# Optimization experiments

Hardware: AMD Instinct MI355X
Metric: run time of the kernel (lower is better)

The kernel has to match this reference:

```python
import jax, jax.numpy as jnp
import numpy as np

HIDDEN = 64
N_NODES = 100000
N_EDGES = 1250000
EDGE_FEAT = 13


def setup_inputs() -> dict:
    key = jax.random.key(0)
    ks = jax.random.split(key, 16)
    d = HIDDEN
    inp = {
        'x': jax.random.normal(ks[0], (N_NODES, d), dtype=jnp.float32),
        'edge_index': jax.random.randint(ks[1], (2, N_EDGES), 0, N_NODES, dtype=jnp.int64),
        'edge_attr': jax.random.uniform(ks[2], (N_EDGES, EDGE_FEAT), dtype=jnp.float32),
        # learned params
        'aaaaa': jax.random.normal(ks[3], (EDGE_FEAT, 1), dtype=jnp.float32) * 0.5,
        'W1': jax.random.normal(ks[4], (d, d), dtype=jnp.float32) / np.sqrt(d),
        'b1': jnp.zeros((d,), dtype=jnp.float32),
        'W2': jax.random.normal(ks[5], (d, d), dtype=jnp.float32) / np.sqrt(d),
        'b2': jnp.zeros((d,), dtype=jnp.float32),
        'W3': jax.random.normal(ks[6], (d, d), dtype=jnp.float32) / np.sqrt(d),
        'b3': jnp.zeros((d,), dtype=jnp.float32),
        'wg1': jax.random.normal(ks[7], (d, 1), dtype=jnp.float32) / np.sqrt(d),
        'bg1': jnp.zeros((1,), dtype=jnp.float32),
        'wg2': jax.random.normal(ks[8], (d, 1), dtype=jnp.float32) / np.sqrt(d),
        'bg2': jnp.zeros((1,), dtype=jnp.float32),
        'wg3': jax.random.normal(ks[9], (d, 1), dtype=jnp.float32) / np.sqrt(d),
        'bg3': jnp.zeros((1,), dtype=jnp.float32),
    }
    return inp


def _gcn_norm(edge_index, edge_weight, num_nodes):
    # PyG gcn_norm: add self-loops (weight 1), symmetric deg^{-1/2} normalization
    loop = jnp.arange(num_nodes, dtype=edge_index.dtype)
    rows = jnp.concatenate([edge_index[0], loop])
    cols = jnp.concatenate([edge_index[1], loop])
    w = jnp.concatenate([edge_weight, jnp.ones((num_nodes,), edge_weight.dtype)])
    deg = jax.ops.segment_sum(w, cols, num_segments=num_nodes)
    dinv = jnp.where(deg > 0, jax.lax.rsqrt(jnp.where(deg > 0, deg, 1.0)), 0.0)
    norm = dinv[rows] * w * dinv[cols]
    return rows, cols, norm


def _gcn_layer(x, W, b, rows, cols, norm, num_nodes):
    h = x @ W  # transform first (out_dim == in_dim)
    msg = norm[:, None] * h[rows]          # gather + scale  [E+N, d]
    out = jnp.zeros_like(h).at[cols].add(msg)  # scatter-add aggregation
    return out + b


def _att_pool(x, wg, bg):
    # GlobalAttention with single graph (batch all zeros):
    # gate = sigmoid(Linear(x)); softmax over nodes; weighted sum
    gate = jax.nn.sigmoid(x @ wg + bg)      # [N, 1]
    a = jax.nn.softmax(gate, axis=0)        # softmax over node dim
    return jnp.sum(a * x, axis=0, keepdims=True)  # [1, d]


def reference(x, edge_index, edge_attr, aaaaa, W1, b1, W2, b2, W3, b3,
              wg1, bg1, wg2, bg2, wg3, bg3):
    num_nodes = x.shape[0]
    edge_weight = (edge_attr @ jax.nn.softmax(aaaaa, axis=0)).reshape(-1)  # [E]
    rows, cols, norm = _gcn_norm(edge_index, edge_weight, num_nodes)

    x1 = jax.nn.relu(_gcn_layer(x, W1, b1, rows, cols, norm, num_nodes))
    r1 = _att_pool(x1, wg1, bg1)
    x2 = jax.nn.relu(_gcn_layer(x1, W2, b2, rows, cols, norm, num_nodes))
    r2 = _att_pool(x2, wg2, bg2)
    x3 = jax.nn.relu(_gcn_layer(x2, W3, b3, rows, cols, norm, num_nodes))
    r3 = _att_pool(x3, wg3, bg3)
    return jnp.concatenate([r1, r2, r3], axis=1)  # [1, 3*hidden]
```

## Files before the change

kernel.cpp:

```cpp
#include <hip/hip_runtime.h>
#include <hip/hip_bf16.h>
#include <math.h>

#define HIDDEN    64
#define N_NODES   100000
#define N_EDGES   1250000
#define EDGE_FEAT 13

#define GATHER_BLOCKS 2048
#define GEMM_NB   ((N_NODES + 255) / 256)

#define NBKT    391
#define BCAP    4096
#define A_EPB   512
#define NBLKA   ((N_EDGES + A_EPB - 1) / A_EPB)
#define CPT     ((NBLKA + 255) / 256)

typedef unsigned short bf16_t;
typedef unsigned char  u8;
typedef unsigned short u16;
typedef unsigned int   u32;
typedef unsigned long long u64;
typedef float f32x2 __attribute__((ext_vector_type(2)));

#if defined(__has_builtin)
# if __has_builtin(__builtin_amdgcn_cvt_f32_fp8)
#  define USE_HW_FP8 1
# endif
# if __has_builtin(__builtin_amdgcn_cvt_pk_f32_fp8)
#  define USE_HW_FP8PK 1
# endif
#endif

static __device__ __forceinline__ float bf2f(bf16_t u) {
    union { unsigned int i; float f; } x; x.i = ((unsigned int)u) << 16; return x.f;
}
static __device__ __forceinline__ bf16_t f2bf(float f) {
    union { float f; unsigned int i; } u; u.f = f;
    unsigned int r = u.i + 0x7FFFu + ((u.i >> 16) & 1u);
    return (bf16_t)(r >> 16);
}

static __device__ __forceinline__ u8 f2fp8(float f) {
    union { float f; unsigned int u; } v; v.f = f;
    unsigned int s = (v.u >> 31) << 7;
    unsigned int mag = v.u & 0x7fffffffu;
    if (mag >= 0x43E80000u) return (u8)(s | 0x7Eu);
    if (mag < 0x3C800000u) {
        union { unsigned int u; float f; } t; t.u = mag;
        int qi = (int)rintf(t.f * 512.0f);
        return (u8)(s | (unsigned int)qi);
    }
    unsigned int r = mag + 0x7FFFFu + ((mag >> 20) & 1u);
    unsigned int e8 = (r >> 23) - 120u;
    unsigned int m3 = (r >> 20) & 7u;
    return (u8)(s | (e8 << 3) | m3);
}

static __device__ __forceinline__ float fp8dec(u32 b) {
#ifdef USE_HW_FP8
    return __builtin_amdgcn_cvt_f32_fp8(b, 0);
#else
    u32 m = b & 0x7Fu;
    u32 sgn = (b & 0x80u) << 24;
    union { u32 u; float f; } fn; fn.u = 0x3C000000u + (m << 20);
    float mg = (m < 8u) ? (float)m * (1.0f / 512.0f) : fn.f;
    union { float f; u32 u; } r; r.f = mg; r.u |= sgn;
    return r.f;
#endif
}

static __device__ __forceinline__ void fp8x4dec(u32 w, float* f) {
#ifdef USE_HW_FP8PK
    f32x2 lo = __builtin_amdgcn_cvt_pk_f32_fp8(w, false);
    f32x2 hi = __builtin_amdgcn_cvt_pk_f32_fp8(w, true);
    f[0] = lo.x; f[1] = lo.y; f[2] = hi.x; f[3] = hi.y;
#else
    f[0] = fp8dec(w & 0xFFu);
    f[1] = fp8dec((w >> 8) & 0xFFu);
    f[2] = fp8dec((w >> 16) & 0xFFu);
    f[3] = fp8dec((w >> 24) & 0xFFu);
#endif
}

#define OFF_TOT    0
#define OFF_GBASE  2048
#define OFF_BLKH   4096
#define OFF_BLKE   3824640
#define OFF_VST    7645184
#define OFF_START  7645184
#define OFF_DINV   8045184
#define OFF_ACC    8445184
#define OFF_POOLP  8446208
#define OFF_REC    10043648
#define OFF_H8     17645184
#define OFF_A      24045184
#define OFF_BREC   OFF_H8

__global__ __launch_bounds__(256) void wqk_kernel(
    const float* __restrict__ attr, const int* __restrict__ rows,
    const int* __restrict__ cols, const float* __restrict__ aaaaa,
    u64* __restrict__ vstash, int* __restrict__ blkHist, int E)
{
    __shared__ float s[16];
    __shared__ int hist[NBKT];
    __shared__ float astage[4][EDGE_FEAT * 64];
    int t = threadIdx.x, blk = blockIdx.x;
    int lane = t & 63, wid = t >> 6;
    if (t == 0) {
        float m = -1e30f;
        for (int i = 0; i < EDGE_FEAT; i++) m = fmaxf(m, aaaaa[i]);
        float ex[EDGE_FEAT]; float sum = 0.f;
        for (int i = 0; i < EDGE_FEAT; i++) { ex[i] = __expf(aaaaa[i] - m); sum += ex[i]; }
        float inv = 1.f / sum;
        for (int i = 0; i < EDGE_FEAT; i++) s[i] = ex[i] * inv;
    }
    for (int b = t; b < NBKT; b += 256) hist[b] = 0;
    __syncthreads();

    float sw[EDGE_FEAT];
#pragma unroll
    for (int f = 0; f < EDGE_FEAT; f++) sw[f] = s[f];

    float* as = astage[wid];
    int wbase = blk * A_EPB + wid * (A_EPB / 4);
#pragma unroll 1
    for (int c = 0; c < A_EPB / 4 / 64; c++) {
        int ebase = wbase + c * 64;
        int rem = E - ebase;
        if (rem <= 0) break;
        int limw = min(64, rem) * EDGE_FEAT;
        size_t gb = (size_t)ebase * EDGE_FEAT;
#pragma unroll
        for (int j = 0; j < EDGE_FEAT; j++) {
            int idx = lane + j * 64;
            if (idx < limw) as[idx] = attr[gb + idx];
        }
        int e = ebase + lane;
        if (e < E) {
            const float* rowp = &as[lane * EDGE_FEAT];
            float acc = 0.f;
#pragma unroll
            for (int f = 0; f < EDGE_FEAT; f++) acc = fmaf(rowp[f], sw[f], acc);
            u32 wq = min((u32)(fmaxf(acc, 0.f) * 32768.0f), 32767u);
            u32 cc = (u32)cols[e], rr = (u32)rows[e];
            int rk = atomicAdd(&hist[cc >> 8], 1);
            vstash[e] = ((u64)(u32)rk << 49) | ((u64)wq << 34) | ((u64)cc << 17) | (u64)rr;
        }
    }
    __syncthreads();
    for (int b = t; b < NBKT; b += 256) blkHist[blk * NBKT + b] = hist[b];
}

__global__ __launch_bounds__(256) void colscan_kernel(
    const int* __restrict__ blkHist, int* __restrict__ blkExcl,
    int* __restrict__ bucketTot)
{
    __shared__ int sc[256];
    int t = threadIdx.x, b = blockIdx.x;
    int loc[CPT]; int lsum = 0;
#pragma unroll
    for (int i = 0; i < CPT; i++) {
        int k = t * CPT + i;
        int v = (k < NBLKA) ? blkHist[(size_t)k * NBKT + b] : 0;
        loc[i] = lsum; lsum += v;
    }
    sc[t] = lsum;
    __syncthreads();
    for (int off = 1; off < 256; off <<= 1) {
        int a = (t >= off) ? sc[t - off] : 0;
        __syncthreads();
        sc[t] += a;
        __syncthreads();
    }
    int excl = sc[t] - lsum;
#pragma unroll
    for (int i = 0; i < CPT; i++) {
        int k = t * CPT + i;
        if (k < NBLKA) blkExcl[(size_t)k * NBKT + b] = excl + loc[i];
    }
    if (t == 255) bucketTot[b] = sc[255];
}

__global__ void bscan(const int* __restrict__ bucketTot, int* __restrict__ gbase) {
    __shared__ int sc[512];
    int t = threadIdx.x;
    int v0 = (t < NBKT) ? bucketTot[t] : 0;
    int v1 = (t + 256 < NBKT) ? bucketTot[t + 256] : 0;
    sc[t] = v0; sc[t + 256] = v1;
    __syncthreads();
    for (int off = 1; off < 512; off <<= 1) {
        int a0 = (t >= off) ? sc[t - off] : 0;
        int a1 = sc[t + 256 - off];
        __syncthreads();
        sc[t] += a0; sc[t + 256] += a1;
        __syncthreads();
    }
    if (t < NBKT) gbase[t] = sc[t] - v0;
    if (t + 256 < NBKT) gbase[t + 256] = sc[t + 256] - v1;
}

__global__ __launch_bounds__(256) void scat_kernel(
    const u64* __restrict__ vstash, const int* __restrict__ blkHist,
    const int* __restrict__ blkExcl, u64* __restrict__ brec, int E)
{
    __shared__ u64 lbuf[A_EPB];
    __shared__ int hist[NBKT];
    __shared__ int exg[NBKT];
    __shared__ int cex[512];
    int t = threadIdx.x, blk = blockIdx.x;
    for (int b = t; b < NBKT; b += 256) {
        hist[b] = blkHist[(size_t)blk * NBKT + b];
        exg[b]  = blkExcl[(size_t)blk * NBKT + b];
    }
    __syncthreads();
    cex[t]       = (t < NBKT) ? hist[t] : 0;
    cex[t + 256] = (t + 256 < NBKT) ? hist[t + 256] : 0;
    __syncthreads();
    for (int off = 1; off < 512; off <<= 1) {
        int a0 = (t >= off) ? cex[t - off] : 0;
        int a1 = cex[t + 256 - off];
        __syncthreads();
        cex[t] += a0; cex[t + 256] += a1;
        __syncthreads();
    }

    int e0 = blk * A_EPB;
    int blkcnt = min(A_EPB, E - e0);
    for (int c = 0; c < A_EPB / 256; c++) {
        int e = e0 + c * 256 + t;
        if (e < E) {
            u64 v = vstash[e];
            int b = (int)((v >> 25) & 0x1FFu);
            int rk = (int)(v >> 49);
            lbuf[cex[b] - hist[b] + rk] = v;
        }
    }
    __syncthreads();
    for (int i = t; i < blkcnt; i += 256) {
        u64 w = lbuf[i];
        int b = (int)((w >> 25) & 0x1FFu);
        int ex = cex[b] - hist[b];
        int slot = exg[b] + (i - ex);
        if (slot < BCAP)
            brec[(size_t)b * BCAP + slot] = w;
    }
}

__global__ __launch_bounds__(256) void sortb_kernel(
    const u64* __restrict__ brec,
    const int* __restrict__ bucketTot, const int* __restrict__ gbase,
    u32* __restrict__ recp, int* __restrict__ startA,
    float* __restrict__ dinv, int N)
{
    __shared__ int hist[256];
    __shared__ int isum[256];
    __shared__ int incl[256];
    __shared__ u16 rnk[BCAP];
    __shared__ u64 buf[BCAP];
    int t = threadIdx.x;
    int b = blockIdx.x;
    int cnt = min(bucketTot[b], BCAP);
    int gb = gbase[b];
    int cbase = b << 8;
    int ncols = min(256, N - cbase);
    hist[t] = 0; isum[t] = 0;
    __syncthreads();

    for (int i = t; i < cnt; i += 256) {
        u64 v = brec[(size_t)b * BCAP + i];
        buf[i] = v;
        int c = (int)((v >> 17) & 255u);
        int wq = (int)((v >> 34) & 0x7FFFu);
        rnk[i] = (u16)atomicAdd(&hist[c], 1);
        atomicAdd(&isum[c], wq);
    }
    __syncthreads();

    incl[t] = hist[t];
    __syncthreads();
    for (int off = 1; off < 256; off <<= 1) {
        int a0 = (t >= off) ? incl[t - off] : 0;
        __syncthreads();
        incl[t] += a0;
        __syncthreads();
    }
    if (t < ncols) {
        startA[cbase + t] = gb + (incl[t] - hist[t]);
        dinv[cbase + t] = rsqrtf(1.0f + (float)isum[t] * (1.0f / 32768.0f));
    }
    __syncthreads();

    for (int i = t; i < cnt; i += 256) {
        u64 v = buf[i];
        int c = (int)((v >> 17) & 255u);
        int ex = incl[c] - hist[c];
        u32 row = (u32)(v & 0x1FFFFu);
        u32 wq = (u32)((v >> 34) & 0x7FFFu);
        recp[gb + ex + rnk[i]] = (row << 15) | wq;
    }
}

template <typename T> struct Feat;
template <> struct Feat<float> {
    static __device__ __forceinline__ float4 ld4(const float* A, size_t off) {
        return *(const float4*)(A + off);
    }
};
template <> struct Feat<bf16_t> {
    static __device__ __forceinline__ float4 ld4(const bf16_t* A, size_t off) {
        uint2 v = *(const uint2*)(A + off);
        float4 r;
        r.x = bf2f((bf16_t)(v.x & 0xffffu));
        r.y = bf2f((bf16_t)(v.x >> 16));
        r.z = bf2f((bf16_t)(v.y & 0xffffu));
        r.w = bf2f((bf16_t)(v.y >> 16));
        return r;
    }
};

template <typename TIn>
__global__ __launch_bounds__(256) void gemm64(const TIn* __restrict__ A,
                                              const float* __restrict__ W,
                                              const float* __restrict__ dinv,
                                              u8* __restrict__ H8, int N) {
    __shared__ float Ws[HIDDEN * HIDDEN];
    int tid = threadIdx.x;
    {
        const float4* Wv = (const float4*)W;
        float4* Sv = (float4*)Ws;
#pragma unroll
        for (int i = 0; i < 4; i++) Sv[tid + 256 * i] = Wv[tid + 256 * i];
    }
    __syncthreads();
    int rg = tid >> 2;
    int c0 = (tid & 3) * 16;
    int rbase = blockIdx.x * 256 + rg;
    int rld[4]; bool rok[4];
#pragma unroll
    for (int i = 0; i < 4; i++) {
        int r = rbase + 64 * i;
        rok[i] = (r < N);
        rld[i] = rok[i] ? r : 0;
    }
    float acc[4][16];
#pragma unroll
    for (int i = 0; i < 4; i++)
#pragma unroll
        for (int j = 0; j < 16; j++) acc[i][j] = 0.f;

    for (int k = 0; k < HIDDEN; k += 4) {
        float4 a4[4];
#pragma unroll
        for (int i = 0; i < 4; i++)
            a4[i] = Feat<TIn>::ld4(A, (size_t)rld[i] * HIDDEN + k);
#pragma unroll
        for (int kk = 0; kk < 4; kk++) {
            const float* wr = &Ws[(k + kk) * HIDDEN + c0];
            float4 W0 = *(const float4*)(wr);
            float4 W1 = *(const float4*)(wr + 4);
            float4 W2 = *(const float4*)(wr + 8);
            float4 W3 = *(const float4*)(wr + 12);
            float wv[16] = {W0.x, W0.y, W0.z, W0.w, W1.x, W1.y, W1.z, W1.w,
                            W2.x, W2.y, W2.z, W2.w, W3.x, W3.y, W3.z, W3.w};
#pragma unroll
            for (int i = 0; i < 4; i++) {
                float ak[4] = {a4[i].x, a4[i].y, a4[i].z, a4[i].w};
                float av = ak[kk];
#pragma unroll
                for (int j = 0; j < 16; j++) acc[i][j] = fmaf(av, wv[j], acc[i][j]);
            }
        }
    }
#pragma unroll
    for (int i = 0; i < 4; i++) {
        if (!rok[i]) continue;
        float dv = dinv[rld[i]];
        unsigned int wd[4];
#pragma unroll
        for (int q = 0; q < 4; q++) {
            unsigned int b0 = f2fp8(dv * acc[i][4*q]);
            unsigned int b1 = f2fp8(dv * acc[i][4*q+1]);
            unsigned int b2 = f2fp8(dv * acc[i][4*q+2]);
            unsigned int b3 = f2fp8(dv * acc[i][4*q+3]);
            wd[q] = b0 | (b1 << 8) | (b2 << 16) | (b3 << 24);
        }
        *(uint4*)(H8 + (size_t)rld[i] * HIDDEN + c0) = make_uint4(wd[0], wd[1], wd[2], wd[3]);
    }
}

__global__ __launch_bounds__(256) void gather_pool_kernel(
    const u8* __restrict__ h8,
    const int* __restrict__ start,
    const u32* __restrict__ recp,
    const float* __restrict__ dinv, const float* __restrict__ bias,
    const float* __restrict__ wg, const float* __restrict__ bg,
    bf16_t* __restrict__ out, float* __restrict__ poolpart, int N)
{
    __shared__ float sred[4][65];
    int lane  = threadIdx.x & 63;
    int wid   = threadIdx.x >> 6;
    int eslot = lane >> 4;
    int ch4   = (lane & 15) * 4;
    int wave = blockIdx.x * 4 + wid;
    const int nwaves = GATHER_BLOCKS * 4;
    float4 wgv = *(const float4*)(wg + ch4);
    float4 bv4 = *(const float4*)(bias + ch4);
    float bg0 = bg[0];
    float accv[4] = {0.f, 0.f, 0.f, 0.f};
    float accs = 0.f;

    for (int n = wave; n < N; n += nwaves) {
        int s = start[n];
        int e2 = (n + 1 < N) ? start[n + 1] : N_EDGES;
        float di = dinv[n];
        float a[4] = {0.f, 0.f, 0.f, 0.f};
        for (int base = s; base < e2; base += 64) {
            int cnt64 = min(e2 - base, 64);
            u32 rv = recp[base + min(lane, cnt64 - 1)];
            for (int j = 0; j < cnt64; j += 8) {
                int q0 = j + eslot, q1 = j + 4 + eslot;
                u32 p0 = (u32)__shfl((int)rv, q0 & 63, 64);
                u32 p1 = (u32)__shfl((int)rv, q1 & 63, 64);
                float w0 = (q0 < cnt64) ? (float)(p0 & 0x7FFFu) : 0.f;
                float w1 = (q1 < cnt64) ? (float)(p1 & 0x7FFFu) : 0.f;
                u32 off0 = ((p0 & 0xFFFF8000u) >> 9) + (u32)ch4;
                u32 off1 = ((p1 & 0xFFFF8000u) >> 9) + (u32)ch4;
                u32 d0 = *(const u32*)(h8 + off0);
                u32 d1 = *(const u32*)(h8 + off1);
                float h0[4], h1[4];
                fp8x4dec(d0, h0);
                fp8x4dec(d1, h1);
#pragma unroll
                for (int i = 0; i < 4; i++) {
                    a[i] = fmaf(w0, h0[i], a[i]);
                    a[i] = fmaf(w1, h1[i], a[i]);
                }
            }
        }
#pragma unroll
        for (int i = 0; i < 4; i++) {
            a[i] += __shfl_xor(a[i], 16, 64);
            a[i] += __shfl_xor(a[i], 32, 64);
        }
        u32 sw = *(const u32*)(h8 + (u32)n * (u32)HIDDEN + (u32)ch4);
        float sf[4];
        fp8x4dec(sw, sf);
        float dis = di * (1.0f / 32768.0f);
        float v[4];
#pragma unroll
        for (int i = 0; i < 4; i++) {
            float t0 = fmaf(dis, a[i], ((const float*)&bv4)[i]);
            v[i] = fmaxf(fmaf(di, sf[i], t0), 0.f);
        }
        if (eslot == 0) {
            u32 lo = (u32)f2bf(v[0]) | ((u32)f2bf(v[1]) << 16);
            u32 hi = (u32)f2bf(v[2]) | ((u32)f2bf(v[3]) << 16);
            *(uint2*)(out + (size_t)n * HIDDEN + ch4) = make_uint2(lo, hi);
        }
        float p = v[0] * wgv.x + v[1] * wgv.y + v[2] * wgv.z + v[3] * wgv.w;
        p += __shfl_xor(p, 1, 64);
        p += __shfl_xor(p, 2, 64);
        p += __shfl_xor(p, 4, 64);
        p += __shfl_xor(p, 8, 64);
        float g = 1.f / (1.f + __expf(-(p + bg0)));
        float eg = __expf(g);
#pragma unroll
        for (int i = 0; i < 4; i++) accv[i] = fmaf(eg, v[i], accv[i]);
        accs += eg;
    }

    if (eslot == 0) {
        sred[wid][ch4 + 0] = accv[0];
        sred[wid][ch4 + 1] = accv[1];
        sred[wid][ch4 + 2] = accv[2];
        sred[wid][ch4 + 3] = accv[3];
    }
    if (lane == 0) sred[wid][64] = accs;
    __syncthreads();
    if (wid == 0) {
        float s0 = sred[0][lane] + sred[1][lane] + sred[2][lane] + sred[3][lane];
        poolpart[(size_t)lane * GATHER_BLOCKS + blockIdx.x] = s0;
        if (lane == 0) {
            float ss = sred[0][64] + sred[1][64] + sred[2][64] + sred[3][64];
            poolpart[(size_t)64 * GATHER_BLOCKS + blockIdx.x] = ss;
        }
    }
}

__global__ void pool_reduce(const float* __restrict__ poolpart, float* __restrict__ acc) {
    int entry = (int)((blockIdx.x * blockDim.x + threadIdx.x) >> 6);
    int lane = threadIdx.x & 63;
    if (entry >= 3 * 65) return;
    const float* p = poolpart + (size_t)entry * GATHER_BLOCKS;
    float s = 0.f;
    for (int i = lane; i < GATHER_BLOCKS; i += 64) s += p[i];
#pragma unroll
    for (int m = 32; m > 0; m >>= 1) s += __shfl_xor(s, m, 64);
    if (lane == 0) acc[entry] = s;
}

__global__ void finalize_kernel(const float* __restrict__ acc, float* __restrict__ out) {
    int i = threadIdx.x;
    if (i >= 3 * HIDDEN) return;
    int layer = i >> 6, c = i & 63;
    const float* a = acc + layer * 65;
    out[i] = a[c] / a[64];
}

extern "C" void kernel_launch(void* const* d_in, const int* in_sizes, int n_in,
                              void* d_out, int out_size, void* d_ws, size_t ws_size,
                              hipStream_t stream) {
    const float* x          = (const float*)d_in[0];
    const int*   edge_index = (const int*)  d_in[1];
    const float* edge_attr  = (const float*)d_in[2];
    const float* aaaaa      = (const float*)d_in[3];
    const float* W1 = (const float*)d_in[4];  const float* b1 = (const float*)d_in[5];
    const float* W2 = (const float*)d_in[6];  const float* b2 = (const float*)d_in[7];
    const float* W3 = (const float*)d_in[8];  const float* b3 = (const float*)d_in[9];
    const float* wg1 = (const float*)d_in[10]; const float* bg1 = (const float*)d_in[11];
    const float* wg2 = (const float*)d_in[12]; const float* bg2 = (const float*)d_in[13];
    const float* wg3 = (const float*)d_in[14]; const float* bg3 = (const float*)d_in[15];
    float* out = (float*)d_out;

    char* ws = (char*)d_ws;
    int*    bucketTot = (int*)   (ws + OFF_TOT);
    int*    gbase     = (int*)   (ws + OFF_GBASE);
    int*    blkHist   = (int*)   (ws + OFF_BLKH);
    int*    blkExcl   = (int*)   (ws + OFF_BLKE);
    u64*    vstash    = (u64*)   (ws + OFF_VST);
    int*    startA    = (int*)   (ws + OFF_START);
    float*  dinv      = (float*) (ws + OFF_DINV);
    float*  acc       = (float*) (ws + OFF_ACC);
    float*  poolpart  = (float*) (ws + OFF_POOLP);
    u32*    recp      = (u32*)   (ws + OFF_REC);
    u8*     h8        = (u8*)    (ws + OFF_H8);
    bf16_t* bufA      = (bf16_t*)(ws + OFF_A);
    u64*    brec      = (u64*)   (ws + OFF_BREC);

    const int* rows = edge_index;
    const int* cols = edge_index + N_EDGES;
    const int N = N_NODES, E = N_EDGES;

    wqk_kernel<<<NBLKA, 256, 0, stream>>>(edge_attr, rows, cols, aaaaa, vstash, blkHist, E);
    colscan_kernel<<<NBKT, 256, 0, stream>>>(blkHist, blkExcl, bucketTot);
    bscan<<<1, 256, 0, stream>>>(bucketTot, gbase);
    scat_kernel<<<NBLKA, 256, 0, stream>>>(vstash, blkHist, blkExcl, brec, E);
    sortb_kernel<<<NBKT, 256, 0, stream>>>(brec, bucketTot, gbase, recp, startA, dinv, N);

    const float* Wm[3]  = {W1, W2, W3};
    const float* bs[3]  = {b1, b2, b3};
    const float* wgs[3] = {wg1, wg2, wg3};
    const float* bgs[3] = {bg1, bg2, bg3};

    for (int l = 0; l < 3; l++) {
        if (l == 0)
            gemm64<float><<<GEMM_NB, 256, 0, stream>>>(x, Wm[l], dinv, h8, N);
        else
            gemm64<bf16_t><<<GEMM_NB, 256, 0, stream>>>(bufA, Wm[l], dinv, h8, N);
        gather_pool_kernel<<<GATHER_BLOCKS, 256, 0, stream>>>(
            h8, startA, recp, dinv, bs[l], wgs[l], bgs[l],
            bufA, poolpart + (size_t)l * 65 * GATHER_BLOCKS, N);
    }

    pool_reduce<<<(3 * 65 * 64 + 255) / 256, 256, 0, stream>>>(poolpart, acc);
    finalize_kernel<<<1, 192, 0, stream>>>(acc, out);
}
```

Baseline: 404.3 us.

## Shrink gemm64 tile to 64 rows per block with 4 columns per thread

```diff
diff --git a/kernel.cpp b/kernel.cpp
--- a/kernel.cpp
+++ b/kernel.cpp
@@ -8,7 +8,8 @@
 #define EDGE_FEAT 13
 
 #define GATHER_BLOCKS 2048
-#define GEMM_NB   ((N_NODES + 255) / 256)
+#define GEMM_ROWS 64
+#define GEMM_NB   ((N_NODES + GEMM_ROWS - 1) / GEMM_ROWS)
 
 #define NBKT    391
 #define BCAP    4096
@@ -333,21 +334,21 @@
         for (int i = 0; i < 4; i++) Sv[tid + 256 * i] = Wv[tid + 256 * i];
     }
     __syncthreads();
-    int rg = tid >> 2;
-    int c0 = (tid & 3) * 16;
-    int rbase = blockIdx.x * 256 + rg;
+    int rg = tid >> 4;
+    int c0 = (tid & 15) * 4;
+    int rbase = blockIdx.x * GEMM_ROWS + rg;
     int rld[4]; bool rok[4];
 #pragma unroll
     for (int i = 0; i < 4; i++) {
-        int r = rbase + 64 * i;
+        int r = rbase + 16 * i;
         rok[i] = (r < N);
         rld[i] = rok[i] ? r : 0;
     }
-    float acc[4][16];
+    float acc[4][4];
 #pragma unroll
     for (int i = 0; i < 4; i++)
 #pragma unroll
-        for (int j = 0; j < 16; j++) acc[i][j] = 0.f;
+        for (int j = 0; j < 4; j++) acc[i][j] = 0.f;
 
     for (int k = 0; k < HIDDEN; k += 4) {
         float4 a4[4];
@@ -356,19 +357,14 @@
             a4[i] = Feat<TIn>::ld4(A, (size_t)rld[i] * HIDDEN + k);
 #pragma unroll
         for (int kk = 0; kk < 4; kk++) {
-            const float* wr = &Ws[(k + kk) * HIDDEN + c0];
-            float4 W0 = *(const float4*)(wr);
-            float4 W1 = *(const float4*)(wr + 4);
-            float4 W2 = *(const float4*)(wr + 8);
-            float4 W3 = *(const float4*)(wr + 12);
-            float wv[16] = {W0.x, W0.y, W0.z, W0.w, W1.x, W1.y, W1.z, W1.w,
-                            W2.x, W2.y, W2.z, W2.w, W3.x, W3.y, W3.z, W3.w};
+            float4 w4 = *(const float4*)(&Ws[(k + kk) * HIDDEN + c0]);
+            float wv[4] = {w4.x, w4.y, w4.z, w4.w};
 #pragma unroll
             for (int i = 0; i < 4; i++) {
                 float ak[4] = {a4[i].x, a4[i].y, a4[i].z, a4[i].w};
                 float av = ak[kk];
 #pragma unroll
-                for (int j = 0; j < 16; j++) acc[i][j] = fmaf(av, wv[j], acc[i][j]);
+                for (int j = 0; j < 4; j++) acc[i][j] = fmaf(av, wv[j], acc[i][j]);
             }
         }
     }
@@ -376,16 +372,12 @@
     for (int i = 0; i < 4; i++) {
         if (!rok[i]) continue;
         float dv = dinv[rld[i]];
-        unsigned int wd[4];
-#pragma unroll
-        for (int q = 0; q < 4; q++) {
-            unsigned int b0 = f2fp8(dv * acc[i][4*q]);
-            unsigned int b1 = f2fp8(dv * acc[i][4*q+1]);
-            unsigned int b2 = f2fp8(dv * acc[i][4*q+2]);
-            unsigned int b3 = f2fp8(dv * acc[i][4*q+3]);
-            wd[q] = b0 | (b1 << 8) | (b2 << 16) | (b3 << 24);
-        }
-        *(uint4*)(H8 + (size_t)rld[i] * HIDDEN + c0) = make_uint4(wd[0], wd[1], wd[2], wd[3]);
+        unsigned int b0 = f2fp8(dv * acc[i][0]);
+        unsigned int b1 = f2fp8(dv * acc[i][1]);
+        unsigned int b2 = f2fp8(dv * acc[i][2]);
+        unsigned int b3 = f2fp8(dv * acc[i][3]);
+        *(u32*)(H8 + (size_t)rld[i] * HIDDEN + c0) =
+            b0 | (b1 << 8) | (b2 << 16) | (b3 << 24);
     }
 }
 
```

Result: no change. 399.3 us (-1.2%).
